# Kernel optimization log

Measured on AMD Instinct MI355X. Metric: run time of the kernel, lower is better.

The kernel has to match this reference:

```python
import jax, jax.numpy as jnp
import numpy as np

N_NODES = 50000
N_EDGES = 800000
N_FEAT = 128
N_HID = 64


def setup_inputs() -> dict:
    key = jax.random.key(0)
    k1, k2, k3, k4, k5, k6, k7 = jax.random.split(key, 7)
    x = jax.random.normal(k1, (N_NODES, N_FEAT), dtype=jnp.float32)
    edge_index = jax.random.randint(k2, (2, N_EDGES), 0, N_NODES, dtype=jnp.int64)
    edge_weight = jax.random.uniform(k3, (N_EDGES,), dtype=jnp.float32)
    # GraphConvolution params (Glorot-ish scaling)
    w1 = jax.random.normal(k4, (N_FEAT, N_HID), dtype=jnp.float32) / np.sqrt(N_FEAT)
    b1 = jnp.zeros((N_HID,), dtype=jnp.float32)
    w2 = jax.random.normal(k5, (N_HID, N_HID), dtype=jnp.float32) / np.sqrt(N_HID)
    b2 = jnp.zeros((N_HID,), dtype=jnp.float32)
    return {"x": x, "edge_index": edge_index, "edge_weight": edge_weight,
            "w1": w1, "b1": b1, "w2": w2, "b2": b2}


def _gcn_layer(h, src, dst, edge_weight, w, b, n_nodes):
    # GraphConvolution: adj @ (h @ w) + b, adj given as weighted edge list
    hw = h @ w                                   # [N, H]
    msgs = hw[src] * edge_weight[:, None]        # [E, H] gather + scale
    agg = jax.ops.segment_sum(msgs, dst, num_segments=n_nodes)  # [N, H]
    return agg + b


def reference(x, edge_index, edge_weight, w1, b1, w2, b2):
    src, dst = edge_index[0], edge_index[1]
    h = jax.nn.relu(_gcn_layer(x, src, dst, edge_weight, w1, b1, N_NODES))
    # dropout is identity in eval mode
    out = _gcn_layer(h, src, dst, edge_weight, w2, b2, N_NODES)
    return out
```

## Files before the change

kernel.cpp:

```cpp
#include <hip/hip_runtime.h>

#define N_NODES 50000
#define N_EDGES 800000
#define N_FEAT  128
#define N_HID   64

#define BKT_LOG 9
#define BKT_SZ  512
#define NBKT    ((N_NODES + BKT_SZ - 1) / BKT_SZ)
#define CH      4096
#define NB1     ((N_EDGES + CH - 1) / CH)
#define GROWS   64
#define GG      ((N_NODES + GROWS - 1) / GROWS)
#define AGG_B   2048

__device__ inline void fma4(float4& acc, float s, const float4& w) {
    acc.x = fmaf(s, w.x, acc.x);
    acc.y = fmaf(s, w.y, acc.y);
    acc.z = fmaf(s, w.z, acc.z);
    acc.w = fmaf(s, w.w, acc.w);
}

__device__ inline unsigned short f2bf(float f) {
    unsigned u = __float_as_uint(f);
    u = u + 0x7FFFu + ((u >> 16) & 1u);
    return (unsigned short)(u >> 16);
}
__device__ inline float bf2f(unsigned short v) { return __uint_as_float(((unsigned)v) << 16); }

__device__ inline int wave_incl_scan(int v) {
    int lane = threadIdx.x & 63;
#pragma unroll
    for (int o = 1; o < 64; o <<= 1) {
        int u = __shfl_up(v, o);
        if (lane >= o) v += u;
    }
    return v;
}

template <int K>
__device__ inline void gemm_body(const float* __restrict__ a, const float* __restrict__ lw,
                                 unsigned short* __restrict__ o, int blk) {
    int tid = threadIdx.x;
    int rp = tid >> 3;
    int c0 = (tid & 7) * 8;
    int row0 = blk * GROWS + rp * 2;
    if (row0 >= N_NODES) return;
    bool two = (row0 + 1) < N_NODES;

    const float* a0 = a + (long)row0 * K;
    const float* a1 = two ? (a0 + K) : a0;

    float4 aA0 = make_float4(0.f, 0.f, 0.f, 0.f), aA1 = aA0;
    float4 aB0 = aA0, aB1 = aA0;

#pragma unroll 4
    for (int k4 = 0; k4 < K / 4; ++k4) {
        float4 xa = *(const float4*)(a0 + k4 * 4);
        float4 xb = *(const float4*)(a1 + k4 * 4);
#pragma unroll
        for (int j = 0; j < 4; ++j) {
            const float* wk = &lw[(k4 * 4 + j) * N_HID + c0];
            float4 w0 = *(const float4*)(wk);
            float4 w1 = *(const float4*)(wk + 4);
            float sa = (j == 0) ? xa.x : (j == 1) ? xa.y : (j == 2) ? xa.z : xa.w;
            float sb = (j == 0) ? xb.x : (j == 1) ? xb.y : (j == 2) ? xb.z : xb.w;
            fma4(aA0, sa, w0); fma4(aA1, sa, w1);
            fma4(aB0, sb, w0); fma4(aB1, sb, w1);
        }
    }

    unsigned short* op = o + (long)row0 * N_HID + c0;
    *(ushort4*)op = make_ushort4(f2bf(aA0.x), f2bf(aA0.y), f2bf(aA0.z), f2bf(aA0.w));
    *(ushort4*)(op + 4) = make_ushort4(f2bf(aA1.x), f2bf(aA1.y), f2bf(aA1.z), f2bf(aA1.w));
    if (two) {
        *(ushort4*)(op + N_HID) = make_ushort4(f2bf(aB0.x), f2bf(aB0.y), f2bf(aB0.z), f2bf(aB0.w));
        *(ushort4*)(op + N_HID + 4) = make_ushort4(f2bf(aB1.x), f2bf(aB1.y), f2bf(aB1.z), f2bf(aB1.w));
    }
}

__global__ __launch_bounds__(256) void gemm1_hist(const float* __restrict__ a,
                                                  const float* __restrict__ w,
                                                  unsigned short* __restrict__ o,
                                                  const int* __restrict__ dst,
                                                  int* __restrict__ cnt,
                                                  int* __restrict__ cnt_t) {
    __shared__ float lw[N_FEAT * N_HID];
    int tid = threadIdx.x;
    if (blockIdx.x < NB1) {
        int* h = (int*)lw;
        int bid = blockIdx.x;
        if (tid < NBKT) h[tid] = 0;
        __syncthreads();
        int e0 = bid * CH;
        for (int i = tid; i < CH; i += 256) {
            int e = e0 + i;
            if (e < N_EDGES) atomicAdd(&h[dst[e] >> BKT_LOG], 1);
        }
        __syncthreads();
        if (tid < NBKT) {
            int v = h[tid];
            cnt[bid * NBKT + tid] = v;
            cnt_t[tid * NB1 + bid] = v;
        }
        return;
    }
    for (int idx = tid * 4; idx < N_FEAT * N_HID; idx += 256 * 4)
        *(float4*)&lw[idx] = *(const float4*)&w[idx];
    __syncthreads();
    gemm_body<N_FEAT>(a, lw, o, blockIdx.x - NB1);
}

template <int K>
__global__ __launch_bounds__(256) void gemm_tile(const float* __restrict__ a,
                                                 const float* __restrict__ w,
                                                 unsigned short* __restrict__ o) {
    __shared__ float lw[K * N_HID];
    int tid = threadIdx.x;
    for (int idx = tid * 4; idx < K * N_HID; idx += 256 * 4)
        *(float4*)&lw[idx] = *(const float4*)&w[idx];
    __syncthreads();
    gemm_body<K>(a, lw, o, blockIdx.x);
}

__global__ __launch_bounds__(256) void binscatter(const int* __restrict__ src,
                                                  const int* __restrict__ dst,
                                                  const float* __restrict__ ew,
                                                  const int* __restrict__ cnt,
                                                  const int* __restrict__ cnt_t,
                                                  uint2* __restrict__ slab) {
    __shared__ int cur[NBKT];
    __shared__ int wtot[2];
    int t = threadIdx.x;
    int b = blockIdx.x;

    int tot = 0, pre = 0;
    if (t < NBKT) {
        const int4* p = (const int4*)(cnt_t + t * NB1);
        for (int q = 0; q < NB1 / 4; ++q) {
            int4 v = p[q];
            tot += v.x + v.y + v.z + v.w;
        }
        int p0 = 0, p1 = 0, p2 = 0, p3 = 0;
        int j = 0;
        for (; j + 4 <= b; j += 4) {
            p0 += cnt[(j + 0) * NBKT + t];
            p1 += cnt[(j + 1) * NBKT + t];
            p2 += cnt[(j + 2) * NBKT + t];
            p3 += cnt[(j + 3) * NBKT + t];
        }
        for (; j < b; ++j) p0 += cnt[j * NBKT + t];
        pre = p0 + p1 + p2 + p3;
    }
    int incl = wave_incl_scan(tot);
    if (t < 128 && (t & 63) == 63) wtot[t >> 6] = incl;
    __syncthreads();
    if (t < NBKT) {
        int bstart_t = (t >= 64 ? wtot[0] : 0) + incl - tot;
        cur[t] = bstart_t + pre;
    }
    __syncthreads();

    int e0 = b * CH;
    for (int i = t; i < CH; i += 256) {
        int e = e0 + i;
        if (e >= N_EDGES) continue;
        int d = dst[e];
        int bin = d >> BKT_LOG;
        int p = atomicAdd(&cur[bin], 1);
        slab[p] = make_uint2((unsigned)src[e] | ((unsigned)(d & (BKT_SZ - 1)) << 16),
                             __float_as_uint(ew[e]));
    }
}

__global__ __launch_bounds__(512) void sort_bucket(const uint2* __restrict__ slab,
                                                   const int* __restrict__ cnt_t,
                                                   unsigned* __restrict__ edges,
                                                   int* __restrict__ start) {
    __shared__ int tt[NBKT];
    __shared__ int h[BKT_SZ];
    __shared__ int wtot[8];
    __shared__ int bs[2];
    int b = blockIdx.x;
    int t = threadIdx.x;
    int lane = t & 63;
    int w = t >> 6;

    if (t < NBKT) {
        int s = 0;
        const int4* p = (const int4*)(cnt_t + t * NB1);
        for (int q = 0; q < NB1 / 4; ++q) {
            int4 v = p[q];
            s += v.x + v.y + v.z + v.w;
        }
        tt[t] = s;
    }
    __syncthreads();
    if (t < 64) {
        int v = (t < b ? tt[t] : 0) + (t + 64 < b ? tt[t + 64] : 0);
#pragma unroll
        for (int o = 32; o >= 1; o >>= 1) v += __shfl_xor(v, o);
        if (t == 0) { bs[0] = v; bs[1] = tt[b]; }
    }
    __syncthreads();
    int base = bs[0];
    int c = bs[1];

    h[t] = 0;
    __syncthreads();
    for (int i = t; i < c; i += 512)
        atomicAdd(&h[(slab[base + i].x >> 16) & (BKT_SZ - 1)], 1);
    __syncthreads();

    int v = h[t];
    int incl = wave_incl_scan(v);
    if (lane == 63) wtot[w] = incl;
    __syncthreads();
    int add = 0;
#pragma unroll
    for (int i = 0; i < 8; ++i) add += (i < w) ? wtot[i] : 0;
    int excl = add + incl - v;

    int g = (b << BKT_LOG) + t;
    if (g < N_NODES) start[g] = base + excl;
    if (b == NBKT - 1 && t == 0) start[N_NODES] = N_EDGES;

    h[t] = base + excl;
    __syncthreads();
    for (int i = t; i < c; i += 512) {
        uint2 r = slab[base + i];
        int p = atomicAdd(&h[(r.x >> 16) & (BKT_SZ - 1)], 1);
        edges[p] = (r.x & 0xFFFFu) | ((unsigned)f2bf(__uint_as_float(r.y)) << 16);
    }
}

__device__ inline float4 agg_core(const unsigned short* __restrict__ hwb,
                                  const unsigned* __restrict__ edges,
                                  int i0, int i1, int es, int f4) {
    float4 acc = make_float4(0.f, 0.f, 0.f, 0.f);
    for (int base = i0; base < i1; base += 16) {
        int ia = base + es;
        int ib = base + 4 + es;
        int ic = base + 8 + es;
        int id = base + 12 + es;
        float wa = 0.f, wb = 0.f, wc = 0.f, wd = 0.f;
        float4 va = make_float4(0.f, 0.f, 0.f, 0.f);
        float4 vb = va, vc = va, vd = va;
        if (ia < i1) {
            unsigned e = edges[ia];
            wa = __uint_as_float(e & 0xFFFF0000u);
            ushort4 v = *(const ushort4*)&hwb[(long)(e & 0xFFFFu) * N_HID + f4];
            va = make_float4(bf2f(v.x), bf2f(v.y), bf2f(v.z), bf2f(v.w));
        }
        if (ib < i1) {
            unsigned e = edges[ib];
            wb = __uint_as_float(e & 0xFFFF0000u);
            ushort4 v = *(const ushort4*)&hwb[(long)(e & 0xFFFFu) * N_HID + f4];
            vb = make_float4(bf2f(v.x), bf2f(v.y), bf2f(v.z), bf2f(v.w));
        }
        if (ic < i1) {
            unsigned e = edges[ic];
            wc = __uint_as_float(e & 0xFFFF0000u);
            ushort4 v = *(const ushort4*)&hwb[(long)(e & 0xFFFFu) * N_HID + f4];
            vc = make_float4(bf2f(v.x), bf2f(v.y), bf2f(v.z), bf2f(v.w));
        }
        if (id < i1) {
            unsigned e = edges[id];
            wd = __uint_as_float(e & 0xFFFF0000u);
            ushort4 v = *(const ushort4*)&hwb[(long)(e & 0xFFFFu) * N_HID + f4];
            vd = make_float4(bf2f(v.x), bf2f(v.y), bf2f(v.z), bf2f(v.w));
        }
        fma4(acc, wa, va);
        fma4(acc, wb, vb);
        fma4(acc, wc, vc);
        fma4(acc, wd, vd);
    }
    acc.x += __shfl_xor(acc.x, 16); acc.y += __shfl_xor(acc.y, 16);
    acc.z += __shfl_xor(acc.z, 16); acc.w += __shfl_xor(acc.w, 16);
    acc.x += __shfl_xor(acc.x, 32); acc.y += __shfl_xor(acc.y, 32);
    acc.z += __shfl_xor(acc.z, 32); acc.w += __shfl_xor(acc.w, 32);
    return acc;
}

__global__ __launch_bounds__(256) void agg_relu(const unsigned short* __restrict__ hwb,
                                                const unsigned* __restrict__ edges,
                                                const int* __restrict__ start,
                                                const float* __restrict__ b1,
                                                float* __restrict__ h) {
    int tid = threadIdx.x;
    int lane = tid & 63;
    int es = lane >> 4;
    int f4 = (lane & 15) * 4;
    float4 bias = *(const float4*)&b1[f4];
    for (int n = blockIdx.x * 4 + (tid >> 6); n < N_NODES; n += AGG_B * 4) {
        float4 acc = agg_core(hwb, edges, start[n], start[n + 1], es, f4);
        if (es == 0) {
            acc.x = fmaxf(acc.x + bias.x, 0.f);
            acc.y = fmaxf(acc.y + bias.y, 0.f);
            acc.z = fmaxf(acc.z + bias.z, 0.f);
            acc.w = fmaxf(acc.w + bias.w, 0.f);
            *(float4*)&h[(long)n * N_HID + f4] = acc;
        }
    }
}

__global__ __launch_bounds__(256) void agg_out(const unsigned short* __restrict__ hwb2,
                                               const unsigned* __restrict__ edges,
                                               const int* __restrict__ start,
                                               const float* __restrict__ b2,
                                               float* __restrict__ o) {
    int tid = threadIdx.x;
    int lane = tid & 63;
    int es = lane >> 4;
    int f4 = (lane & 15) * 4;
    float4 bias = *(const float4*)&b2[f4];
    for (int n = blockIdx.x * 4 + (tid >> 6); n < N_NODES; n += AGG_B * 4) {
        float4 acc = agg_core(hwb2, edges, start[n], start[n + 1], es, f4);
        if (es == 0) {
            acc.x += bias.x; acc.y += bias.y; acc.z += bias.z; acc.w += bias.w;
            *(float4*)&o[(long)n * N_HID + f4] = acc;
        }
    }
}

extern "C" void kernel_launch(void* const* d_in, const int* in_sizes, int n_in,
                              void* d_out, int out_size, void* d_ws, size_t ws_size,
                              hipStream_t stream) {
    const float* x  = (const float*)d_in[0];
    const int*   ei = (const int*)d_in[1];
    const float* ew = (const float*)d_in[2];
    const float* w1 = (const float*)d_in[3];
    const float* b1 = (const float*)d_in[4];
    const float* w2 = (const float*)d_in[5];
    const float* b2 = (const float*)d_in[6];
    float* out = (float*)d_out;

    const int* src = ei;
    const int* dst = ei + N_EDGES;

    char* ws = (char*)d_ws;
    unsigned short* hwb  = (unsigned short*)ws;
    unsigned short* hwb2 = (unsigned short*)(ws + (size_t)7  * 1024 * 1024);
    uint2*    slab  = (uint2*)   (ws + (size_t)14 * 1024 * 1024);
    unsigned* edges = (unsigned*)(ws + (size_t)21 * 1024 * 1024);
    int*      start = (int*)     (ws + (size_t)25 * 1024 * 1024);
    int*      cnt   = start + N_NODES + 8;
    int*      cnt_t = cnt + NB1 * NBKT;

    dim3 blk(256);

    gemm1_hist<<<dim3(NB1 + GG), blk, 0, stream>>>(x, w1, hwb, dst, cnt, cnt_t);
    binscatter<<<dim3(NB1), blk, 0, stream>>>(src, dst, ew, cnt, cnt_t, slab);
    sort_bucket<<<dim3(NBKT), dim3(512), 0, stream>>>(slab, cnt_t, edges, start);
    agg_relu<<<dim3(AGG_B), blk, 0, stream>>>(hwb, edges, start, b1, out);
    gemm_tile<N_HID><<<dim3(GG), blk, 0, stream>>>(out, w2, hwb2);
    agg_out<<<dim3(AGG_B), blk, 0, stream>>>(hwb2, edges, start, b2, out);
}
```

Before: 127.8 us.

## Fuse layer-1 aggregation with layer-2 GEMM to skip hidden activation round trip

The first-layer aggregation kernel now computes each node's ReLU'd hidden row in shared memory. The same wavefront then immediately multiplies it by a swizzled, transposed copy of w2 held in LDS, writing bf16 hw2 directly. This removes the fp32 hidden-activation write and re-read through global memory, and drops the separate gemm_tile launch. In exchange, every node pays a per-wave 64x64 matvec from LDS inside the gather loop, which adds LDS traffic and ALU work to a latency-bound kernel.

```diff
diff --git a/kernel.cpp b/kernel.cpp
--- a/kernel.cpp
+++ b/kernel.cpp
@@ -111,18 +111,6 @@
     gemm_body<N_FEAT>(a, lw, o, blockIdx.x - NB1);
 }
 
-template <int K>
-__global__ __launch_bounds__(256) void gemm_tile(const float* __restrict__ a,
-                                                 const float* __restrict__ w,
-                                                 unsigned short* __restrict__ o) {
-    __shared__ float lw[K * N_HID];
-    int tid = threadIdx.x;
-    for (int idx = tid * 4; idx < K * N_HID; idx += 256 * 4)
-        *(float4*)&lw[idx] = *(const float4*)&w[idx];
-    __syncthreads();
-    gemm_body<K>(a, lw, o, blockIdx.x);
-}
-
 __global__ __launch_bounds__(256) void binscatter(const int* __restrict__ src,
                                                   const int* __restrict__ dst,
                                                   const float* __restrict__ ew,
@@ -282,25 +270,51 @@
     return acc;
 }
 
-__global__ __launch_bounds__(256) void agg_relu(const unsigned short* __restrict__ hwb,
-                                                const unsigned* __restrict__ edges,
-                                                const int* __restrict__ start,
-                                                const float* __restrict__ b1,
-                                                float* __restrict__ h) {
+__global__ __launch_bounds__(256) void agg1_gemm2(const unsigned short* __restrict__ hwb,
+                                                  const unsigned* __restrict__ edges,
+                                                  const int* __restrict__ start,
+                                                  const float* __restrict__ b1,
+                                                  const float* __restrict__ w2,
+                                                  unsigned short* __restrict__ hwb2) {
+    __shared__ float lw2t[N_HID * N_HID];
+    __shared__ float hrow[4][N_HID];
     int tid = threadIdx.x;
+    for (int idx = tid; idx < N_HID * N_HID; idx += 256) {
+        int k = idx >> 6, c = idx & 63;
+        lw2t[c * N_HID + (k ^ ((c & 7) << 2))] = w2[idx];
+    }
+    __syncthreads();
+
     int lane = tid & 63;
+    int wv = tid >> 6;
     int es = lane >> 4;
     int f4 = (lane & 15) * 4;
     float4 bias = *(const float4*)&b1[f4];
-    for (int n = blockIdx.x * 4 + (tid >> 6); n < N_NODES; n += AGG_B * 4) {
+    const float* colp = &lw2t[lane * N_HID];
+    int swz = (lane & 7) << 2;
+
+    for (int n = blockIdx.x * 4 + wv; n < N_NODES; n += AGG_B * 4) {
         float4 acc = agg_core(hwb, edges, start[n], start[n + 1], es, f4);
         if (es == 0) {
             acc.x = fmaxf(acc.x + bias.x, 0.f);
             acc.y = fmaxf(acc.y + bias.y, 0.f);
             acc.z = fmaxf(acc.z + bias.z, 0.f);
             acc.w = fmaxf(acc.w + bias.w, 0.f);
-            *(float4*)&h[(long)n * N_HID + f4] = acc;
-        }
+            *(float4*)&hrow[wv][f4] = acc;
+        }
+        float oa = 0.f, ob = 0.f;
+#pragma unroll
+        for (int k4 = 0; k4 < N_HID / 4; k4 += 2) {
+            float4 h0 = *(const float4*)&hrow[wv][k4 * 4];
+            float4 h1 = *(const float4*)&hrow[wv][k4 * 4 + 4];
+            float4 w0 = *(const float4*)&colp[(k4 * 4) ^ swz];
+            float4 w1 = *(const float4*)&colp[(k4 * 4 + 4) ^ swz];
+            oa = fmaf(h0.x, w0.x, oa); oa = fmaf(h0.y, w0.y, oa);
+            oa = fmaf(h0.z, w0.z, oa); oa = fmaf(h0.w, w0.w, oa);
+            ob = fmaf(h1.x, w1.x, ob); ob = fmaf(h1.y, w1.y, ob);
+            ob = fmaf(h1.z, w1.z, ob); ob = fmaf(h1.w, w1.w, ob);
+        }
+        hwb2[(long)n * N_HID + lane] = f2bf(oa + ob);
     }
 }
 
@@ -352,7 +366,6 @@
     gemm1_hist<<<dim3(NB1 + GG), blk, 0, stream>>>(x, w1, hwb, dst, cnt, cnt_t);
     binscatter<<<dim3(NB1), blk, 0, stream>>>(src, dst, ew, cnt, cnt_t, slab);
     sort_bucket<<<dim3(NBKT), dim3(512), 0, stream>>>(slab, cnt_t, edges, start);
-    agg_relu<<<dim3(AGG_B), blk, 0, stream>>>(hwb, edges, start, b1, out);
-    gemm_tile<N_HID><<<dim3(GG), blk, 0, stream>>>(out, w2, hwb2);
+    agg1_gemm2<<<dim3(AGG_B), blk, 0, stream>>>(hwb, edges, start, b1, w2, hwb2);
     agg_out<<<dim3(AGG_B), blk, 0, stream>>>(hwb2, edges, start, b2, out);
 }
```

New measurement: 143.7 us. 12.4% more time.

## Widen aggregation gathers to 16-byte bf16 rows and store hidden layer as bf16

Applied to the files above, without the earlier changes.

The aggregation kernels now have each lane gather 8 bf16 features with one 16-byte load, so 8 edges are in flight per step instead of 4, and the shuffle reduction gains one more level. The first layer's ReLU output is written as bf16 into a new workspace buffer, and a dedicated second GEMM reads bf16 input directly. This halves the intermediate write and read traffic and cuts gather instruction count, at the cost of extra rounding on the hidden activations and fewer edges per lane per iteration.

```diff
diff --git a/kernel.cpp b/kernel.cpp
--- a/kernel.cpp
+++ b/kernel.cpp
@@ -26,7 +26,6 @@
     u = u + 0x7FFFu + ((u >> 16) & 1u);
     return (unsigned short)(u >> 16);
 }
-__device__ inline float bf2f(unsigned short v) { return __uint_as_float(((unsigned)v) << 16); }
 
 __device__ inline int wave_incl_scan(int v) {
     int lane = threadIdx.x & 63;
@@ -36,6 +35,17 @@
         if (lane >= o) v += u;
     }
     return v;
+}
+
+__device__ inline void fma_bf8(float4& lo, float4& hi, float w, const uint4& v) {
+    lo.x = fmaf(w, __uint_as_float(v.x << 16), lo.x);
+    lo.y = fmaf(w, __uint_as_float(v.x & 0xFFFF0000u), lo.y);
+    lo.z = fmaf(w, __uint_as_float(v.y << 16), lo.z);
+    lo.w = fmaf(w, __uint_as_float(v.y & 0xFFFF0000u), lo.w);
+    hi.x = fmaf(w, __uint_as_float(v.z << 16), hi.x);
+    hi.y = fmaf(w, __uint_as_float(v.z & 0xFFFF0000u), hi.y);
+    hi.z = fmaf(w, __uint_as_float(v.w << 16), hi.z);
+    hi.w = fmaf(w, __uint_as_float(v.w & 0xFFFF0000u), hi.w);
 }
 
 template <int K>
@@ -111,16 +121,57 @@
     gemm_body<N_FEAT>(a, lw, o, blockIdx.x - NB1);
 }
 
-template <int K>
-__global__ __launch_bounds__(256) void gemm_tile(const float* __restrict__ a,
-                                                 const float* __restrict__ w,
-                                                 unsigned short* __restrict__ o) {
-    __shared__ float lw[K * N_HID];
+__global__ __launch_bounds__(256) void gemm2_bf16(const unsigned short* __restrict__ a,
+                                                  const float* __restrict__ w,
+                                                  unsigned short* __restrict__ o) {
+    __shared__ float lw[N_HID * N_HID];
     int tid = threadIdx.x;
-    for (int idx = tid * 4; idx < K * N_HID; idx += 256 * 4)
+    for (int idx = tid * 4; idx < N_HID * N_HID; idx += 256 * 4)
         *(float4*)&lw[idx] = *(const float4*)&w[idx];
     __syncthreads();
-    gemm_body<K>(a, lw, o, blockIdx.x);
+
+    int rp = tid >> 3;
+    int c0 = (tid & 7) * 8;
+    int row0 = blockIdx.x * GROWS + rp * 2;
+    if (row0 >= N_NODES) return;
+    bool two = (row0 + 1) < N_NODES;
+
+    const unsigned short* a0 = a + (long)row0 * N_HID;
+    const unsigned short* a1 = two ? (a0 + N_HID) : a0;
+
+    float4 aA0 = make_float4(0.f, 0.f, 0.f, 0.f), aA1 = aA0;
+    float4 aB0 = aA0, aB1 = aA0;
+
+#pragma unroll 2
+    for (int k8 = 0; k8 < N_HID / 8; ++k8) {
+        uint4 xa = *(const uint4*)(a0 + k8 * 8);
+        uint4 xb = *(const uint4*)(a1 + k8 * 8);
+        float sa[8], sb[8];
+        sa[0] = __uint_as_float(xa.x << 16); sa[1] = __uint_as_float(xa.x & 0xFFFF0000u);
+        sa[2] = __uint_as_float(xa.y << 16); sa[3] = __uint_as_float(xa.y & 0xFFFF0000u);
+        sa[4] = __uint_as_float(xa.z << 16); sa[5] = __uint_as_float(xa.z & 0xFFFF0000u);
+        sa[6] = __uint_as_float(xa.w << 16); sa[7] = __uint_as_float(xa.w & 0xFFFF0000u);
+        sb[0] = __uint_as_float(xb.x << 16); sb[1] = __uint_as_float(xb.x & 0xFFFF0000u);
+        sb[2] = __uint_as_float(xb.y << 16); sb[3] = __uint_as_float(xb.y & 0xFFFF0000u);
+        sb[4] = __uint_as_float(xb.z << 16); sb[5] = __uint_as_float(xb.z & 0xFFFF0000u);
+        sb[6] = __uint_as_float(xb.w << 16); sb[7] = __uint_as_float(xb.w & 0xFFFF0000u);
+#pragma unroll
+        for (int j = 0; j < 8; ++j) {
+            const float* wk = &lw[(k8 * 8 + j) * N_HID + c0];
+            float4 w0 = *(const float4*)(wk);
+            float4 w1 = *(const float4*)(wk + 4);
+            fma4(aA0, sa[j], w0); fma4(aA1, sa[j], w1);
+            fma4(aB0, sb[j], w0); fma4(aB1, sb[j], w1);
+        }
+    }
+
+    unsigned short* op = o + (long)row0 * N_HID + c0;
+    *(ushort4*)op = make_ushort4(f2bf(aA0.x), f2bf(aA0.y), f2bf(aA0.z), f2bf(aA0.w));
+    *(ushort4*)(op + 4) = make_ushort4(f2bf(aA1.x), f2bf(aA1.y), f2bf(aA1.z), f2bf(aA1.w));
+    if (two) {
+        *(ushort4*)(op + N_HID) = make_ushort4(f2bf(aB0.x), f2bf(aB0.y), f2bf(aB0.z), f2bf(aB0.w));
+        *(ushort4*)(op + N_HID + 4) = make_ushort4(f2bf(aB1.x), f2bf(aB1.y), f2bf(aB1.z), f2bf(aB1.w));
+    }
 }
 
 __global__ __launch_bounds__(256) void binscatter(const int* __restrict__ src,
@@ -234,72 +285,64 @@
     }
 }
 
-__device__ inline float4 agg_core(const unsigned short* __restrict__ hwb,
-                                  const unsigned* __restrict__ edges,
-                                  int i0, int i1, int es, int f4) {
-    float4 acc = make_float4(0.f, 0.f, 0.f, 0.f);
+__device__ inline void agg_core8(const unsigned short* __restrict__ hwb,
+                                 const unsigned* __restrict__ edges,
+                                 int i0, int i1, int es, int f8,
+                                 float4& lo, float4& hi) {
+    lo = make_float4(0.f, 0.f, 0.f, 0.f);
+    hi = lo;
     for (int base = i0; base < i1; base += 16) {
         int ia = base + es;
-        int ib = base + 4 + es;
-        int ic = base + 8 + es;
-        int id = base + 12 + es;
-        float wa = 0.f, wb = 0.f, wc = 0.f, wd = 0.f;
-        float4 va = make_float4(0.f, 0.f, 0.f, 0.f);
-        float4 vb = va, vc = va, vd = va;
+        int ib = base + 8 + es;
+        float wa = 0.f, wb = 0.f;
+        uint4 va = make_uint4(0u, 0u, 0u, 0u), vb = va;
         if (ia < i1) {
             unsigned e = edges[ia];
             wa = __uint_as_float(e & 0xFFFF0000u);
-            ushort4 v = *(const ushort4*)&hwb[(long)(e & 0xFFFFu) * N_HID + f4];
-            va = make_float4(bf2f(v.x), bf2f(v.y), bf2f(v.z), bf2f(v.w));
+            va = *(const uint4*)&hwb[(long)(e & 0xFFFFu) * N_HID + f8];
         }
         if (ib < i1) {
             unsigned e = edges[ib];
             wb = __uint_as_float(e & 0xFFFF0000u);
-            ushort4 v = *(const ushort4*)&hwb[(long)(e & 0xFFFFu) * N_HID + f4];
-            vb = make_float4(bf2f(v.x), bf2f(v.y), bf2f(v.z), bf2f(v.w));
-        }
-        if (ic < i1) {
-            unsigned e = edges[ic];
-            wc = __uint_as_float(e & 0xFFFF0000u);
-            ushort4 v = *(const ushort4*)&hwb[(long)(e & 0xFFFFu) * N_HID + f4];
-            vc = make_float4(bf2f(v.x), bf2f(v.y), bf2f(v.z), bf2f(v.w));
-        }
-        if (id < i1) {
-            unsigned e = edges[id];
-            wd = __uint_as_float(e & 0xFFFF0000u);
-            ushort4 v = *(const ushort4*)&hwb[(long)(e & 0xFFFFu) * N_HID + f4];
-            vd = make_float4(bf2f(v.x), bf2f(v.y), bf2f(v.z), bf2f(v.w));
-        }
-        fma4(acc, wa, va);
-        fma4(acc, wb, vb);
-        fma4(acc, wc, vc);
-        fma4(acc, wd, vd);
-    }
-    acc.x += __shfl_xor(acc.x, 16); acc.y += __shfl_xor(acc.y, 16);
-    acc.z += __shfl_xor(acc.z, 16); acc.w += __shfl_xor(acc.w, 16);
-    acc.x += __shfl_xor(acc.x, 32); acc.y += __shfl_xor(acc.y, 32);
-    acc.z += __shfl_xor(acc.z, 32); acc.w += __shfl_xor(acc.w, 32);
-    return acc;
+            vb = *(const uint4*)&hwb[(long)(e & 0xFFFFu) * N_HID + f8];
+        }
+        fma_bf8(lo, hi, wa, va);
+        fma_bf8(lo, hi, wb, vb);
+    }
+#pragma unroll
+    for (int m = 8; m <= 32; m <<= 1) {
+        lo.x += __shfl_xor(lo.x, m); lo.y += __shfl_xor(lo.y, m);
+        lo.z += __shfl_xor(lo.z, m); lo.w += __shfl_xor(lo.w, m);
+        hi.x += __shfl_xor(hi.x, m); hi.y += __shfl_xor(hi.y, m);
+        hi.z += __shfl_xor(hi.z, m); hi.w += __shfl_xor(hi.w, m);
+    }
 }
 
 __global__ __launch_bounds__(256) void agg_relu(const unsigned short* __restrict__ hwb,
                                                 const unsigned* __restrict__ edges,
                                                 const int* __restrict__ start,
                                                 const float* __restrict__ b1,
-                                                float* __restrict__ h) {
+                                                unsigned short* __restrict__ hb) {
     int tid = threadIdx.x;
     int lane = tid & 63;
-    int es = lane >> 4;
-    int f4 = (lane & 15) * 4;
-    float4 bias = *(const float4*)&b1[f4];
+    int es = lane >> 3;
+    int f8 = (lane & 7) * 8;
+    float4 bl = *(const float4*)&b1[f8];
+    float4 bh = *(const float4*)&b1[f8 + 4];
     for (int n = blockIdx.x * 4 + (tid >> 6); n < N_NODES; n += AGG_B * 4) {
-        float4 acc = agg_core(hwb, edges, start[n], start[n + 1], es, f4);
+        float4 lo, hi;
+        agg_core8(hwb, edges, start[n], start[n + 1], es, f8, lo, hi);
         if (es == 0) {
-            acc.x = fmaxf(acc.x + bias.x, 0.f);
-            acc.y = fmaxf(acc.y + bias.y, 0.f);
-            acc.z = fmaxf(acc.z + bias.z, 0.f);
-            acc.w = fmaxf(acc.w + bias.w, 0.f);
-            *(float4*)&h[(long)n * N_HID + f4] = acc;
+            lo.x = fmaxf(lo.x + bl.x, 0.f); lo.y = fmaxf(lo.y + bl.y, 0.f);
+            lo.z = fmaxf(lo.z + bl.z, 0.f); lo.w = fmaxf(lo.w + bl.w, 0.f);
+            hi.x = fmaxf(hi.x + bh.x, 0.f); hi.y = fmaxf(hi.y + bh.y, 0.f);
+            hi.z = fmaxf(hi.z + bh.z, 0.f); hi.w = fmaxf(hi.w + bh.w, 0.f);
+            uint4 p;
+            p.x = (unsigned)f2bf(lo.x) | ((unsigned)f2bf(lo.y) << 16);
+            p.y = (unsigned)f2bf(lo.z) | ((unsigned)f2bf(lo.w) << 16);
+            p.z = (unsigned)f2bf(hi.x) | ((unsigned)f2bf(hi.y) << 16);
+            p.w = (unsigned)f2bf(hi.z) | ((unsigned)f2bf(hi.w) << 16);
+            *(uint4*)&hb[(long)n * N_HID + f8] = p;
         }
     }
 }
@@ -311,14 +354,18 @@
                                                float* __restrict__ o) {
     int tid = threadIdx.x;
     int lane = tid & 63;
-    int es = lane >> 4;
-    int f4 = (lane & 15) * 4;
-    float4 bias = *(const float4*)&b2[f4];
+    int es = lane >> 3;
+    int f8 = (lane & 7) * 8;
+    float4 bl = *(const float4*)&b2[f8];
+    float4 bh = *(const float4*)&b2[f8 + 4];
     for (int n = blockIdx.x * 4 + (tid >> 6); n < N_NODES; n += AGG_B * 4) {
-        float4 acc = agg_core(hwb2, edges, start[n], start[n + 1], es, f4);
+        float4 lo, hi;
+        agg_core8(hwb2, edges, start[n], start[n + 1], es, f8, lo, hi);
         if (es == 0) {
-            acc.x += bias.x; acc.y += bias.y; acc.z += bias.z; acc.w += bias.w;
-            *(float4*)&o[(long)n * N_HID + f4] = acc;
+            lo.x += bl.x; lo.y += bl.y; lo.z += bl.z; lo.w += bl.w;
+            hi.x += bh.x; hi.y += bh.y; hi.z += bh.z; hi.w += bh.w;
+            *(float4*)&o[(long)n * N_HID + f8] = lo;
+            *(float4*)&o[(long)n * N_HID + f8 + 4] = hi;
         }
     }
 }
@@ -341,9 +388,10 @@
     char* ws = (char*)d_ws;
     unsigned short* hwb  = (unsigned short*)ws;
     unsigned short* hwb2 = (unsigned short*)(ws + (size_t)7  * 1024 * 1024);
-    uint2*    slab  = (uint2*)   (ws + (size_t)14 * 1024 * 1024);
-    unsigned* edges = (unsigned*)(ws + (size_t)21 * 1024 * 1024);
-    int*      start = (int*)     (ws + (size_t)25 * 1024 * 1024);
+    unsigned short* hb   = (unsigned short*)(ws + (size_t)14 * 1024 * 1024);
+    uint2*    slab  = (uint2*)   (ws + (size_t)21 * 1024 * 1024);
+    unsigned* edges = (unsigned*)(ws + (size_t)28 * 1024 * 1024);
+    int*      start = (int*)     (ws + (size_t)32 * 1024 * 1024);
     int*      cnt   = start + N_NODES + 8;
     int*      cnt_t = cnt + NB1 * NBKT;
 
@@ -352,7 +400,7 @@
     gemm1_hist<<<dim3(NB1 + GG), blk, 0, stream>>>(x, w1, hwb, dst, cnt, cnt_t);
     binscatter<<<dim3(NB1), blk, 0, stream>>>(src, dst, ew, cnt, cnt_t, slab);
     sort_bucket<<<dim3(NBKT), dim3(512), 0, stream>>>(slab, cnt_t, edges, start);
-    agg_relu<<<dim3(AGG_B), blk, 0, stream>>>(hwb, edges, start, b1, out);
-    gemm_tile<N_HID><<<dim3(GG), blk, 0, stream>>>(out, w2, hwb2);
+    agg_relu<<<dim3(AGG_B), blk, 0, stream>>>(hwb, edges, start, b1, hb);
+    gemm2_bf16<<<dim3(GG), blk, 0, stream>>>(hb, w2, hwb2);
     agg_out<<<dim3(AGG_B), blk, 0, stream>>>(hwb2, edges, start, b2, out);
 }
```

Result: faster. 112.2 us, median of 2 (-12.2%).
